# Kernel tuning notes

Hardware: AMD Instinct MI355X
Metric: run time of the kernel (lower is better)

The kernel has to match this reference:

```python
import jax, jax.numpy as jnp
import numpy as np

B, N, F, A = 8, 2048, 512, 512  # batch, n_dim (tokens), feature_dim, attention_dim
BN_EPS = 1e-5


def setup_inputs() -> dict:
    key = jax.random.key(0)
    ks = jax.random.split(key, 9)
    s_f = 1.0 / np.sqrt(F)
    s_a = 1.0 / np.sqrt(A)
    return {
        "x": jax.random.normal(ks[0], (B, N, F), dtype=jnp.float32),
        "Wq": jax.random.uniform(ks[1], (A, F), jnp.float32, -s_f, s_f),
        "bq": jax.random.uniform(ks[2], (A,), jnp.float32, -s_f, s_f),
        "Wk": jax.random.uniform(ks[3], (A, F), jnp.float32, -s_f, s_f),
        "bk": jax.random.uniform(ks[4], (A,), jnp.float32, -s_f, s_f),
        "Wv": jax.random.uniform(ks[5], (A, F), jnp.float32, -s_f, s_f),
        "bv": jax.random.uniform(ks[6], (A,), jnp.float32, -s_f, s_f),
        "Wo": jax.random.uniform(ks[7], (F, A), jnp.float32, -s_a, s_a),
        "bo": jax.random.uniform(ks[8], (F,), jnp.float32, -s_a, s_a),
        "gamma": jnp.ones((N,), dtype=jnp.float32),
        "beta": jnp.zeros((N,), dtype=jnp.float32),
    }


def reference(x, Wq, bq, Wk, bk, Wv, bv, Wo, bo, gamma, beta):
    # QKV projections: [B,N,F] -> [B,N,A]
    q = jnp.einsum("bnf,af->bna", x, Wq) + bq
    k = jnp.einsum("bnf,af->bna", x, Wk) + bk
    v = jnp.einsum("bnf,af->bna", x, Wv) + bv
    # unscaled single-head attention (no 1/sqrt(d) factor, matches source)
    scores = jnp.einsum("bna,bma->bnm", q, k)          # [B,N,N]
    weights = jax.nn.softmax(scores, axis=-1)
    feature = jnp.einsum("bnm,bma->bna", weights, v)    # [B,N,A]
    # LBR: Linear -> BatchNorm1d(n_dim) over channel dim N -> ReLU
    lin = jnp.einsum("bna,fa->bnf", feature, Wo) + bo   # [B,N,F]
    mean = jnp.mean(lin, axis=(0, 2), keepdims=True)    # stats over batch+last dim
    var = jnp.mean(jnp.square(lin - mean), axis=(0, 2), keepdims=True)  # biased var
    bn = gamma[None, :, None] * (lin - mean) * jax.lax.rsqrt(var + BN_EPS) + beta[None, :, None]
    return jax.nn.relu(bn) + x
```

## Files before the change

### kernel.cpp

```cpp
#include <hip/hip_runtime.h>
#include <hip/hip_fp16.h>
#include <stdint.h>

#define B_   8
#define N_   2048
#define F_   512
#define A_   512
#define MTOT (B_ * N_)

typedef unsigned short u16;
typedef unsigned int   u32;
typedef __attribute__((ext_vector_type(8))) __bf16    bf16x8;
typedef __attribute__((ext_vector_type(8))) _Float16  f16x8;
typedef __attribute__((ext_vector_type(4))) float     f32x4;

__device__ __forceinline__ u16 f2bf(float f) {
    u32 u = __builtin_bit_cast(u32, f);
    u32 r = u + 0x7fffu + ((u >> 16) & 1u);
    return (u16)(r >> 16);
}
__device__ __forceinline__ float bf2f(u16 h) {
    return __builtin_bit_cast(float, (u32)h << 16);
}
__device__ __forceinline__ u16 f2h(float f) {
    _Float16 h = (_Float16)f;
    return __builtin_bit_cast(u16, h);
}

__device__ __forceinline__ void gload_lds16(const u16* g, u16* l) {
    __builtin_amdgcn_global_load_lds(
        (const __attribute__((address_space(1))) u32*)(const u32*)g,
        (__attribute__((address_space(3))) u32*)(u32*)l,
        16, 0, 0);
}

#define VMCNT(n) asm volatile("s_waitcnt vmcnt(" #n ")" ::: "memory")
#define LGKM0()  asm volatile("s_waitcnt lgkmcnt(0)" ::: "memory")
#define SCHEDB() __builtin_amdgcn_sched_barrier(0)

__device__ __forceinline__ void sync_pre() {
    SCHEDB();
    __builtin_amdgcn_s_barrier();
    LGKM0();
    SCHEDB();
}
__device__ __forceinline__ void sync_post() {
    SCHEDB();
    __builtin_amdgcn_s_barrier();
}

__global__ __launch_bounds__(256) void cvt_x(const float* __restrict__ in,
                                             u16* __restrict__ out, int n4) {
    int i = blockIdx.x * 256 + threadIdx.x;
    if (i >= n4) return;
    float4 v = ((const float4*)in)[i];
    u32 a = (u32)f2h(v.x) | ((u32)f2h(v.y) << 16);
    u32 b = (u32)f2h(v.z) | ((u32)f2h(v.w) << 16);
    ((uint2*)out)[i] = make_uint2(a, b);
}

__global__ __launch_bounds__(256)
void cvt_wb(const float* __restrict__ Wq, const float* __restrict__ Wk,
            const float* __restrict__ Wv, const float* __restrict__ Wo,
            const float* __restrict__ bq, const float* __restrict__ bk,
            u16* __restrict__ wqkh, u16* __restrict__ wvh, u16* __restrict__ wob,
            float* __restrict__ bqk)
{
    int b = blockIdx.x, t = threadIdx.x;
    int i = (b & 255) * 256 + t;
    int seg = b >> 8;
    const float* src = seg == 0 ? Wq : seg == 1 ? Wk : seg == 2 ? Wv : Wo;
    u16* dst = seg == 0 ? wqkh : seg == 1 ? (wqkh + 262144) : seg == 2 ? wvh : wob;
    float4 v = ((const float4*)src)[i];
    u32 a, c;
    if (seg < 3) {
        a = (u32)f2h(v.x) | ((u32)f2h(v.y) << 16);
        c = (u32)f2h(v.z) | ((u32)f2h(v.w) << 16);
    } else {
        a = (u32)f2bf(v.x) | ((u32)f2bf(v.y) << 16);
        c = (u32)f2bf(v.z) | ((u32)f2bf(v.w) << 16);
    }
    ((uint2*)dst)[i] = make_uint2(a, c);
    if (b == 0 && t < 128) ((float4*)bqk)[t]         = ((const float4*)bq)[t];
    if (b == 1 && t < 128) ((float4*)(bqk + 512))[t] = ((const float4*)bk)[t];
}

template <int BN, int BIAS_MODE, int OUT_FMT, int IN_FMT, int EPI, int XS>
__global__ __launch_bounds__(512, 2)
void gemm8(const u16* __restrict__ A, int lda, long sA,
           const u16* __restrict__ Bm, int ldb, long sB,
           const float* __restrict__ bias,
           void* __restrict__ Cv, int ldc, long sC, int K, int bdiag,
           float* __restrict__ aux)
{
    constexpr int UNITS = (BN == 256) ? 4 : 3;
    constexpr int NF = BN / 64;
    __shared__ alignas(16) u16 lds[2 * UNITS * 8192];

    int bx = blockIdx.x, bz = blockIdx.z;
    if constexpr (XS == 1) { int tt = bx; bx = bz; bz = tt; }
    if constexpr (XS == 2) { bx = ((bx & 7) << 3) | (bx >> 3); }
    const int z  = bz;
    const int m0 = bx * 256;
    const int n0 = blockIdx.y * BN;
    const u16* Ag = A  + (long)z * sA + (long)m0 * lda;
    const u16* Bg = Bm + (long)z * sB + (long)n0 * ldb + (long)(m0 >> 11) * bdiag;

    const int t = threadIdx.x;
    const int lane = t & 63;
    const int wave = t >> 6;
    const int wm = wave >> 2, wn = wave & 3;
    const int frow = lane & 15;
    const int fk8 = (lane >> 4) * 8;

    const int srr = t >> 3;
    const int ses = ((t & 7) * 8) ^ ((srr & 7) << 3);

    auto stageA = [&](int buf, int h, int kt) {
        u16* dst = &lds[(buf * UNITS + h) * 8192 + t * 8];
        const u16* g = Ag + kt * 64 + ses;
        gload_lds16(g + (long)(srr + h * 64) * lda,        dst);
        gload_lds16(g + (long)(srr + 128 + h * 64) * lda,  dst + 4096);
    };
    auto stageB = [&](int buf, int h, int kt) {
        u16* dst = &lds[(buf * UNITS + 2 + h) * 8192 + t * 8];
        const u16* g = Bg + kt * 64 + ses;
        int R0;
        if constexpr (BN == 256) R0 = (srr & 31) + ((srr >> 5) << 6) + h * 32;
        else                     R0 = srr;
        int R1 = R0 + ((BN == 256) ? 128 : 64);
        gload_lds16(g + (long)R0 * ldb, dst);
        gload_lds16(g + (long)R1 * ldb, dst + 4096);
    };
    auto rdA = [&](int buf, int q, int i, int ks) -> uint4 {
        int rr = wm * 64 + i * 16 + frow;
        int e  = (ks * 32 + fk8) ^ ((rr & 7) << 3);
        return *(const uint4*)&lds[(buf * UNITS + q) * 8192 + rr * 64 + e];
    };
    auto rdB = [&](int buf, int p, int j, int ks) -> uint4 {
        int rr = wn * 32 + j * 16 + frow;
        int e  = (ks * 32 + fk8) ^ ((rr & 7) << 3);
        return *(const uint4*)&lds[(buf * UNITS + 2 + p) * 8192 + rr * 64 + e];
    };
    auto MF = [&](uint4 a, uint4 b, f32x4 c) -> f32x4 {
        if constexpr (IN_FMT == 0)
            return __builtin_amdgcn_mfma_f32_16x16x32_bf16(
                __builtin_bit_cast(bf16x8, a), __builtin_bit_cast(bf16x8, b), c, 0, 0, 0);
        else
            return __builtin_amdgcn_mfma_f32_16x16x32_f16(
                __builtin_bit_cast(f16x8, a), __builtin_bit_cast(f16x8, b), c, 0, 0, 0);
    };

    f32x4 acc[8][NF];
#pragma unroll
    for (int i = 0; i < 8; i++)
#pragma unroll
        for (int j = 0; j < NF; j++)
#pragma unroll
            for (int r = 0; r < 4; r++) acc[i][j][r] = 0.f;

    uint4 fa[4][2], fb0[2][2], fb1[2][2];
    const int NT = K >> 6;

    if constexpr (BN == 256) {
        stageA(0, 0, 0); stageB(0, 0, 0); stageB(0, 1, 0); stageA(0, 1, 0);
        VMCNT(4);
    } else {
        stageA(0, 0, 0); stageB(0, 0, 0); stageA(0, 1, 0);
        VMCNT(2);
    }
    SCHEDB();
    __builtin_amdgcn_s_barrier();

    for (int kt = 0; kt < NT; ++kt) {
        const int buf = kt & 1, nb = buf ^ 1;
        const bool st = (kt + 1 < NT);

        if constexpr (BN == 256) {
#pragma unroll
            for (int i = 0; i < 4; i++) { fa[i][0] = rdA(buf, 0, i, 0); fa[i][1] = rdA(buf, 0, i, 1); }
#pragma unroll
            for (int j = 0; j < 2; j++) { fb0[j][0] = rdB(buf, 0, j, 0); fb0[j][1] = rdB(buf, 0, j, 1); }
            if (st) { stageA(nb, 0, kt + 1); VMCNT(4); } else VMCNT(2);
            sync_pre();
            __builtin_amdgcn_s_setprio(1);
#pragma unroll
            for (int ks = 0; ks < 2; ks++)
#pragma unroll
                for (int i = 0; i < 4; i++)
#pragma unroll
                    for (int j = 0; j < 2; j++)
                        acc[i][j] = MF(fa[i][ks], fb0[j][ks], acc[i][j]);
            __builtin_amdgcn_s_setprio(0);
            sync_post();
#pragma unroll
            for (int j = 0; j < 2; j++) { fb1[j][0] = rdB(buf, 1, j, 0); fb1[j][1] = rdB(buf, 1, j, 1); }
            if (st) { stageB(nb, 0, kt + 1); VMCNT(4); } else VMCNT(0);
            sync_pre();
            __builtin_amdgcn_s_setprio(1);
#pragma unroll
            for (int ks = 0; ks < 2; ks++)
#pragma unroll
                for (int i = 0; i < 4; i++)
#pragma unroll
                    for (int j = 0; j < 2; j++)
                        acc[i][2 + j] = MF(fa[i][ks], fb1[j][ks], acc[i][2 + j]);
            __builtin_amdgcn_s_setprio(0);
            sync_post();
#pragma unroll
            for (int i = 0; i < 4; i++) { fa[i][0] = rdA(buf, 1, i, 0); fa[i][1] = rdA(buf, 1, i, 1); }
            if (st) stageB(nb, 1, kt + 1);
            sync_pre();
            __builtin_amdgcn_s_setprio(1);
#pragma unroll
            for (int ks = 0; ks < 2; ks++)
#pragma unroll
                for (int i = 0; i < 4; i++)
#pragma unroll
                    for (int j = 0; j < 2; j++)
                        acc[4 + i][j] = MF(fa[i][ks], fb0[j][ks], acc[4 + i][j]);
            __builtin_amdgcn_s_setprio(0);
            sync_post();
            if (st) { stageA(nb, 1, kt + 1); VMCNT(4); }
            sync_pre();
            __builtin_amdgcn_s_setprio(1);
#pragma unroll
            for (int ks = 0; ks < 2; ks++)
#pragma unroll
                for (int i = 0; i < 4; i++)
#pragma unroll
                    for (int j = 0; j < 2; j++)
                        acc[4 + i][2 + j] = MF(fa[i][ks], fb1[j][ks], acc[4 + i][2 + j]);
            __builtin_amdgcn_s_setprio(0);
            sync_post();
        } else {
#pragma unroll
            for (int i = 0; i < 4; i++) { fa[i][0] = rdA(buf, 0, i, 0); fa[i][1] = rdA(buf, 0, i, 1); }
#pragma unroll
            for (int j = 0; j < 2; j++) { fb0[j][0] = rdB(buf, 0, j, 0); fb0[j][1] = rdB(buf, 0, j, 1); }
            if (st) { stageA(nb, 0, kt + 1); stageB(nb, 0, kt + 1); VMCNT(4); } else VMCNT(0);
            sync_pre();
            __builtin_amdgcn_s_setprio(1);
#pragma unroll
            for (int ks = 0; ks < 2; ks++)
#pragma unroll
                for (int i = 0; i < 4; i++)
#pragma unroll
                    for (int j = 0; j < 2; j++)
                        acc[i][j] = MF(fa[i][ks], fb0[j][ks], acc[i][j]);
            __builtin_amdgcn_s_setprio(0);
            sync_post();
#pragma unroll
            for (int i = 0; i < 4; i++) { fa[i][0] = rdA(buf, 1, i, 0); fa[i][1] = rdA(buf, 1, i, 1); }
            if (st) { stageA(nb, 1, kt + 1); VMCNT(2); }
            sync_pre();
            __builtin_amdgcn_s_setprio(1);
#pragma unroll
            for (int ks = 0; ks < 2; ks++)
#pragma unroll
                for (int i = 0; i < 4; i++)
#pragma unroll
                    for (int j = 0; j < 2; j++)
                        acc[4 + i][j] = MF(fa[i][ks], fb0[j][ks], acc[4 + i][j]);
            __builtin_amdgcn_s_setprio(0);
            sync_post();
        }
    }

    const int rq = (lane >> 4) * 4;
#pragma unroll
    for (int am = 0; am < 8; am++) {
        const int m = m0 + wm * 128 + (am >> 2) * 64 + (am & 3) * 16 + rq;
#pragma unroll
        for (int r = 0; r < 4; r++) {
            float rscale = 1.f;
            if constexpr (EPI == 3) rscale = 1.0f / aux[m + r];
            float se = 0.f, s1 = 0.f, s2 = 0.f;
#pragma unroll
            for (int an = 0; an < NF; an++) {
                const int n = n0 + wn * (BN / 4) + an * 16 + frow;
                float v = acc[am][an][r];
                if (BIAS_MODE == 1) v += bias[n];
                if (BIAS_MODE == 2) v += bias[m + r];
                if constexpr (EPI == 1) { v = __expf(v); se += v; }
                if constexpr (EPI == 3) { v *= rscale; }
                if constexpr (EPI == 2) { s1 += v; s2 += v * v; }
                long idx = (long)(m + r) * ldc + n + (long)z * sC;
                if constexpr (OUT_FMT == 0)      ((u16*)Cv)[idx] = f2bf(v);
                else if constexpr (OUT_FMT == 1) ((float*)Cv)[idx] = v;
                else                             ((u16*)Cv)[idx] = f2h(v);
            }
            if constexpr (EPI == 1) {
#pragma unroll
                for (int o = 1; o < 16; o <<= 1) se += __shfl_xor(se, o);
                if (frow == 0)
                    atomicAdd(&aux[(long)z * N_ + m + r], se);
            }
            if constexpr (EPI == 2) {
#pragma unroll
                for (int o = 1; o < 16; o <<= 1) { s1 += __shfl_xor(s1, o); s2 += __shfl_xor(s2, o); }
                if (frow == 0) {
                    int tok = (m + r) & (N_ - 1);
                    atomicAdd(&aux[tok], s1);
                    atomicAdd(&aux[N_ + tok], s2);
                }
            }
        }
    }
}

__global__ __launch_bounds__(256)
void bn_relu_add(const u16* __restrict__ linb, const u16* __restrict__ xh,
                 const float* __restrict__ gamma, const float* __restrict__ beta,
                 const float* __restrict__ stats, float* __restrict__ out) {
    long i4 = (long)blockIdx.x * 256 + threadIdx.x;
    int n = (int)((i4 >> 7) & (N_ - 1));
    float mean = stats[n] * (1.f / 4096.f);
    float var  = stats[N_ + n] * (1.f / 4096.f) - mean * mean;
    float rstd = rsqrtf(var + 1e-5f);
    float scale = gamma[n] * rstd;
    float shift = beta[n] - mean * scale;
    uint2 lb = ((const uint2*)linb)[i4];
    uint2 xb = ((const uint2*)xh)[i4];
    float2 x01 = __half22float2(__builtin_bit_cast(__half2, xb.x));
    float2 x23 = __half22float2(__builtin_bit_cast(__half2, xb.y));
    float4 o;
    o.x = fmaxf(bf2f((u16)lb.x)         * scale + shift, 0.f) + x01.x;
    o.y = fmaxf(bf2f((u16)(lb.x >> 16)) * scale + shift, 0.f) + x01.y;
    o.z = fmaxf(bf2f((u16)lb.y)         * scale + shift, 0.f) + x23.x;
    o.w = fmaxf(bf2f((u16)(lb.y >> 16)) * scale + shift, 0.f) + x23.y;
    ((float4*)out)[i4] = o;
}

extern "C" void kernel_launch(void* const* d_in, const int* in_sizes, int n_in,
                              void* d_out, int out_size, void* d_ws, size_t ws_size,
                              hipStream_t stream)
{
    (void)in_sizes; (void)n_in; (void)out_size; (void)ws_size;
    const float* x     = (const float*)d_in[0];
    const float* Wq    = (const float*)d_in[1];
    const float* bq    = (const float*)d_in[2];
    const float* Wk    = (const float*)d_in[3];
    const float* bk    = (const float*)d_in[4];
    const float* Wv    = (const float*)d_in[5];
    const float* bv    = (const float*)d_in[6];
    const float* Wo    = (const float*)d_in[7];
    const float* bo    = (const float*)d_in[8];
    const float* gamma = (const float*)d_in[9];
    const float* beta  = (const float*)d_in[10];
    float* out = (float*)d_out;
    char*  ws  = (char*)d_ws;

    const size_t MB = 1024 * 1024;
    u16*   wqkh  = (u16*)(ws + 0);
    u16*   wvh   = (u16*)(ws + 1 * MB);
    u16*   wob   = (u16*)(ws + 1 * MB + 512 * 1024);
    float* stats = (float*)(ws + 2 * MB);
    float* rowsum= (float*)(ws + 2 * MB + 16 * 1024);
    float* bqk   = (float*)(ws + 2 * MB + 80 * 1024);
    u16*   xh    = (u16*)(ws + 4 * MB);
    u16*   qkh   = (u16*)(ws + 20 * MB);
    u16*   vt    = (u16*)(ws + 52 * MB);
    u16*   P     = (u16*)(ws + 68 * MB);
    u16*   feat  = (u16*)(ws + 132 * MB);
    u16*   lin   = (u16*)(ws + 148 * MB);

    hipMemsetAsync(stats, 0, 80 * 1024, stream);

    cvt_x<<<8192, 256, 0, stream>>>(x, xh, 2097152);
    cvt_wb<<<1024, 256, 0, stream>>>(Wq, Wk, Wv, Wo, bq, bk, wqkh, wvh, wob, bqk);

    gemm8<256, 1, 2, 1, 0, 0><<<dim3(64, 4, 1), 512, 0, stream>>>(
        xh, 512, 0, wqkh, 512, 0, bqk, qkh, 1024, 0, 512, 0, nullptr);
    gemm8<128, 2, 0, 1, 0, 0><<<dim3(2, 128, 1), 512, 0, stream>>>(
        wvh, 512, 0, xh, 512, 0, bv, vt, MTOT, 0, 512, 0, nullptr);
    gemm8<256, 0, 0, 1, 1, 1><<<dim3(8, 8, 8), 512, 0, stream>>>(
        qkh, 1024, (long)N_ * 1024, qkh + 512, 1024, (long)N_ * 1024,
        nullptr, P, N_, (long)N_ * N_, 512, 0, rowsum);
    gemm8<128, 0, 0, 0, 3, 2><<<dim3(64, 4, 1), 512, 0, stream>>>(
        P, N_, 0, vt, MTOT, 0, nullptr, feat, A_, 0, 2048, 2048, rowsum);
    gemm8<128, 1, 0, 0, 2, 0><<<dim3(64, 4, 1), 512, 0, stream>>>(
        feat, 512, 0, wob, 512, 0, bo, lin, 512, 0, 512, 0, stats);

    bn_relu_add<<<8192, 256, 0, stream>>>(lin, xh, gamma, beta, stats, out);
}
```

Baseline: 217.2 us.

## Replace GEMM double-buffer with triple-buffered 256x128 tile pipeline

Replaces the gemm8 template (BN 256 or 128, double-buffered LDS, two barriers per sub-step) with gemm9, which uses only 256x128 tiles and a three-stage LDS ring that prefetches two k-steps ahead. Each k-iteration now needs one barrier instead of several, which is meant to cut sync overhead and hide global-load latency. The QK projection and score GEMMs move from BN=256 to BN=128 with twice the grid in y. That loses some A-tile reuse, and the larger LDS footprint (144KB) plus the dropped min-blocks launch bound reduce occupancy to one block per CU.

```diff
diff --git a/kernel.cpp b/kernel.cpp
--- a/kernel.cpp
+++ b/kernel.cpp
@@ -37,17 +37,6 @@
 #define VMCNT(n) asm volatile("s_waitcnt vmcnt(" #n ")" ::: "memory")
 #define LGKM0()  asm volatile("s_waitcnt lgkmcnt(0)" ::: "memory")
 #define SCHEDB() __builtin_amdgcn_sched_barrier(0)
-
-__device__ __forceinline__ void sync_pre() {
-    SCHEDB();
-    __builtin_amdgcn_s_barrier();
-    LGKM0();
-    SCHEDB();
-}
-__device__ __forceinline__ void sync_post() {
-    SCHEDB();
-    __builtin_amdgcn_s_barrier();
-}
 
 __global__ __launch_bounds__(256) void cvt_x(const float* __restrict__ in,
                                              u16* __restrict__ out, int n4) {
@@ -85,24 +74,22 @@
     if (b == 1 && t < 128) ((float4*)(bqk + 512))[t] = ((const float4*)bk)[t];
 }
 
-template <int BN, int BIAS_MODE, int OUT_FMT, int IN_FMT, int EPI, int XS>
-__global__ __launch_bounds__(512, 2)
-void gemm8(const u16* __restrict__ A, int lda, long sA,
+template <int BIAS_MODE, int OUT_FMT, int IN_FMT, int EPI, int XS>
+__global__ __launch_bounds__(512)
+void gemm9(const u16* __restrict__ A, int lda, long sA,
            const u16* __restrict__ Bm, int ldb, long sB,
            const float* __restrict__ bias,
            void* __restrict__ Cv, int ldc, long sC, int K, int bdiag,
            float* __restrict__ aux)
 {
-    constexpr int UNITS = (BN == 256) ? 4 : 3;
-    constexpr int NF = BN / 64;
-    __shared__ alignas(16) u16 lds[2 * UNITS * 8192];
+    __shared__ alignas(16) u16 lds[9 * 8192];
 
     int bx = blockIdx.x, bz = blockIdx.z;
     if constexpr (XS == 1) { int tt = bx; bx = bz; bz = tt; }
     if constexpr (XS == 2) { bx = ((bx & 7) << 3) | (bx >> 3); }
     const int z  = bz;
     const int m0 = bx * 256;
-    const int n0 = blockIdx.y * BN;
+    const int n0 = blockIdx.y * 128;
     const u16* Ag = A  + (long)z * sA + (long)m0 * lda;
     const u16* Bg = Bm + (long)z * sB + (long)n0 * ldb + (long)(m0 >> 11) * bdiag;
 
@@ -117,30 +104,26 @@
     const int ses = ((t & 7) * 8) ^ ((srr & 7) << 3);
 
     auto stageA = [&](int buf, int h, int kt) {
-        u16* dst = &lds[(buf * UNITS + h) * 8192 + t * 8];
+        u16* dst = &lds[(buf * 3 + h) * 8192 + t * 8];
         const u16* g = Ag + kt * 64 + ses;
         gload_lds16(g + (long)(srr + h * 64) * lda,        dst);
         gload_lds16(g + (long)(srr + 128 + h * 64) * lda,  dst + 4096);
     };
-    auto stageB = [&](int buf, int h, int kt) {
-        u16* dst = &lds[(buf * UNITS + 2 + h) * 8192 + t * 8];
+    auto stageB = [&](int buf, int kt) {
+        u16* dst = &lds[(buf * 3 + 2) * 8192 + t * 8];
         const u16* g = Bg + kt * 64 + ses;
-        int R0;
-        if constexpr (BN == 256) R0 = (srr & 31) + ((srr >> 5) << 6) + h * 32;
-        else                     R0 = srr;
-        int R1 = R0 + ((BN == 256) ? 128 : 64);
-        gload_lds16(g + (long)R0 * ldb, dst);
-        gload_lds16(g + (long)R1 * ldb, dst + 4096);
+        gload_lds16(g + (long)srr * ldb,        dst);
+        gload_lds16(g + (long)(srr + 64) * ldb, dst + 4096);
     };
     auto rdA = [&](int buf, int q, int i, int ks) -> uint4 {
         int rr = wm * 64 + i * 16 + frow;
         int e  = (ks * 32 + fk8) ^ ((rr & 7) << 3);
-        return *(const uint4*)&lds[(buf * UNITS + q) * 8192 + rr * 64 + e];
-    };
-    auto rdB = [&](int buf, int p, int j, int ks) -> uint4 {
+        return *(const uint4*)&lds[(buf * 3 + q) * 8192 + rr * 64 + e];
+    };
+    auto rdB = [&](int buf, int j, int ks) -> uint4 {
         int rr = wn * 32 + j * 16 + frow;
         int e  = (ks * 32 + fk8) ^ ((rr & 7) << 3);
-        return *(const uint4*)&lds[(buf * UNITS + 2 + p) * 8192 + rr * 64 + e];
+        return *(const uint4*)&lds[(buf * 3 + 2) * 8192 + rr * 64 + e];
     };
     auto MF = [&](uint4 a, uint4 b, f32x4 c) -> f32x4 {
         if constexpr (IN_FMT == 0)
@@ -151,120 +134,62 @@
                 __builtin_bit_cast(f16x8, a), __builtin_bit_cast(f16x8, b), c, 0, 0, 0);
     };
 
-    f32x4 acc[8][NF];
+    f32x4 acc[8][2];
 #pragma unroll
     for (int i = 0; i < 8; i++)
 #pragma unroll
-        for (int j = 0; j < NF; j++)
+        for (int j = 0; j < 2; j++)
 #pragma unroll
             for (int r = 0; r < 4; r++) acc[i][j][r] = 0.f;
 
-    uint4 fa[4][2], fb0[2][2], fb1[2][2];
+    uint4 fa[4][2], fb[2][2];
     const int NT = K >> 6;
 
-    if constexpr (BN == 256) {
-        stageA(0, 0, 0); stageB(0, 0, 0); stageB(0, 1, 0); stageA(0, 1, 0);
-        VMCNT(4);
-    } else {
-        stageA(0, 0, 0); stageB(0, 0, 0); stageA(0, 1, 0);
-        VMCNT(2);
-    }
-    SCHEDB();
-    __builtin_amdgcn_s_barrier();
-
+    stageA(0, 0, 0); stageB(0, 0); stageA(0, 1, 0);
+    stageA(1, 0, 1); stageB(1, 1); stageA(1, 1, 1);
+
+    int bR = 0;
     for (int kt = 0; kt < NT; ++kt) {
-        const int buf = kt & 1, nb = buf ^ 1;
-        const bool st = (kt + 1 < NT);
-
-        if constexpr (BN == 256) {
-#pragma unroll
-            for (int i = 0; i < 4; i++) { fa[i][0] = rdA(buf, 0, i, 0); fa[i][1] = rdA(buf, 0, i, 1); }
-#pragma unroll
-            for (int j = 0; j < 2; j++) { fb0[j][0] = rdB(buf, 0, j, 0); fb0[j][1] = rdB(buf, 0, j, 1); }
-            if (st) { stageA(nb, 0, kt + 1); VMCNT(4); } else VMCNT(2);
-            sync_pre();
-            __builtin_amdgcn_s_setprio(1);
-#pragma unroll
-            for (int ks = 0; ks < 2; ks++)
-#pragma unroll
-                for (int i = 0; i < 4; i++)
-#pragma unroll
-                    for (int j = 0; j < 2; j++)
-                        acc[i][j] = MF(fa[i][ks], fb0[j][ks], acc[i][j]);
-            __builtin_amdgcn_s_setprio(0);
-            sync_post();
-#pragma unroll
-            for (int j = 0; j < 2; j++) { fb1[j][0] = rdB(buf, 1, j, 0); fb1[j][1] = rdB(buf, 1, j, 1); }
-            if (st) { stageB(nb, 0, kt + 1); VMCNT(4); } else VMCNT(0);
-            sync_pre();
-            __builtin_amdgcn_s_setprio(1);
-#pragma unroll
-            for (int ks = 0; ks < 2; ks++)
-#pragma unroll
-                for (int i = 0; i < 4; i++)
-#pragma unroll
-                    for (int j = 0; j < 2; j++)
-                        acc[i][2 + j] = MF(fa[i][ks], fb1[j][ks], acc[i][2 + j]);
-            __builtin_amdgcn_s_setprio(0);
-            sync_post();
-#pragma unroll
-            for (int i = 0; i < 4; i++) { fa[i][0] = rdA(buf, 1, i, 0); fa[i][1] = rdA(buf, 1, i, 1); }
-            if (st) stageB(nb, 1, kt + 1);
-            sync_pre();
-            __builtin_amdgcn_s_setprio(1);
-#pragma unroll
-            for (int ks = 0; ks < 2; ks++)
-#pragma unroll
-                for (int i = 0; i < 4; i++)
-#pragma unroll
-                    for (int j = 0; j < 2; j++)
-                        acc[4 + i][j] = MF(fa[i][ks], fb0[j][ks], acc[4 + i][j]);
-            __builtin_amdgcn_s_setprio(0);
-            sync_post();
-            if (st) { stageA(nb, 1, kt + 1); VMCNT(4); }
-            sync_pre();
-            __builtin_amdgcn_s_setprio(1);
-#pragma unroll
-            for (int ks = 0; ks < 2; ks++)
-#pragma unroll
-                for (int i = 0; i < 4; i++)
-#pragma unroll
-                    for (int j = 0; j < 2; j++)
-                        acc[4 + i][2 + j] = MF(fa[i][ks], fb1[j][ks], acc[4 + i][2 + j]);
-            __builtin_amdgcn_s_setprio(0);
-            sync_post();
-        } else {
-#pragma unroll
-            for (int i = 0; i < 4; i++) { fa[i][0] = rdA(buf, 0, i, 0); fa[i][1] = rdA(buf, 0, i, 1); }
-#pragma unroll
-            for (int j = 0; j < 2; j++) { fb0[j][0] = rdB(buf, 0, j, 0); fb0[j][1] = rdB(buf, 0, j, 1); }
-            if (st) { stageA(nb, 0, kt + 1); stageB(nb, 0, kt + 1); VMCNT(4); } else VMCNT(0);
-            sync_pre();
-            __builtin_amdgcn_s_setprio(1);
-#pragma unroll
-            for (int ks = 0; ks < 2; ks++)
-#pragma unroll
-                for (int i = 0; i < 4; i++)
-#pragma unroll
-                    for (int j = 0; j < 2; j++)
-                        acc[i][j] = MF(fa[i][ks], fb0[j][ks], acc[i][j]);
-            __builtin_amdgcn_s_setprio(0);
-            sync_post();
-#pragma unroll
-            for (int i = 0; i < 4; i++) { fa[i][0] = rdA(buf, 1, i, 0); fa[i][1] = rdA(buf, 1, i, 1); }
-            if (st) { stageA(nb, 1, kt + 1); VMCNT(2); }
-            sync_pre();
-            __builtin_amdgcn_s_setprio(1);
-#pragma unroll
-            for (int ks = 0; ks < 2; ks++)
-#pragma unroll
-                for (int i = 0; i < 4; i++)
-#pragma unroll
-                    for (int j = 0; j < 2; j++)
-                        acc[4 + i][j] = MF(fa[i][ks], fb0[j][ks], acc[4 + i][j]);
-            __builtin_amdgcn_s_setprio(0);
-            sync_post();
-        }
+        int bS = bR + 2; if (bS >= 3) bS -= 3;
+        const bool st = (kt + 2 < NT);
+
+        if (kt + 1 < NT) { VMCNT(6); } else { VMCNT(0); }
+        SCHEDB();
+        __builtin_amdgcn_s_barrier();
+        SCHEDB();
+
+        if (st) { stageA(bS, 0, kt + 2); stageB(bS, kt + 2); }
+#pragma unroll
+        for (int i = 0; i < 4; i++) { fa[i][0] = rdA(bR, 0, i, 0); fa[i][1] = rdA(bR, 0, i, 1); }
+#pragma unroll
+        for (int j = 0; j < 2; j++) { fb[j][0] = rdB(bR, j, 0); fb[j][1] = rdB(bR, j, 1); }
+        LGKM0(); SCHEDB();
+        __builtin_amdgcn_s_setprio(1);
+#pragma unroll
+        for (int ks = 0; ks < 2; ks++)
+#pragma unroll
+            for (int i = 0; i < 4; i++)
+#pragma unroll
+                for (int j = 0; j < 2; j++)
+                    acc[i][j] = MF(fa[i][ks], fb[j][ks], acc[i][j]);
+        __builtin_amdgcn_s_setprio(0);
+
+        if (st) stageA(bS, 1, kt + 2);
+#pragma unroll
+        for (int i = 0; i < 4; i++) { fa[i][0] = rdA(bR, 1, i, 0); fa[i][1] = rdA(bR, 1, i, 1); }
+        LGKM0(); SCHEDB();
+        __builtin_amdgcn_s_setprio(1);
+#pragma unroll
+        for (int ks = 0; ks < 2; ks++)
+#pragma unroll
+            for (int i = 0; i < 4; i++)
+#pragma unroll
+                for (int j = 0; j < 2; j++)
+                    acc[4 + i][j] = MF(fa[i][ks], fb[j][ks], acc[4 + i][j]);
+        __builtin_amdgcn_s_setprio(0);
+        SCHEDB();
+
+        bR += 1; if (bR == 3) bR = 0;
     }
 
     const int rq = (lane >> 4) * 4;
@@ -277,8 +202,8 @@
             if constexpr (EPI == 3) rscale = 1.0f / aux[m + r];
             float se = 0.f, s1 = 0.f, s2 = 0.f;
 #pragma unroll
-            for (int an = 0; an < NF; an++) {
-                const int n = n0 + wn * (BN / 4) + an * 16 + frow;
+            for (int an = 0; an < 2; an++) {
+                const int n = n0 + wn * 32 + an * 16 + frow;
                 float v = acc[am][an][r];
                 if (BIAS_MODE == 1) v += bias[n];
                 if (BIAS_MODE == 2) v += bias[m + r];
@@ -370,16 +295,16 @@
     cvt_x<<<8192, 256, 0, stream>>>(x, xh, 2097152);
     cvt_wb<<<1024, 256, 0, stream>>>(Wq, Wk, Wv, Wo, bq, bk, wqkh, wvh, wob, bqk);
 
-    gemm8<256, 1, 2, 1, 0, 0><<<dim3(64, 4, 1), 512, 0, stream>>>(
+    gemm9<1, 2, 1, 0, 0><<<dim3(64, 8, 1), 512, 0, stream>>>(
         xh, 512, 0, wqkh, 512, 0, bqk, qkh, 1024, 0, 512, 0, nullptr);
-    gemm8<128, 2, 0, 1, 0, 0><<<dim3(2, 128, 1), 512, 0, stream>>>(
+    gemm9<2, 0, 1, 0, 0><<<dim3(2, 128, 1), 512, 0, stream>>>(
         wvh, 512, 0, xh, 512, 0, bv, vt, MTOT, 0, 512, 0, nullptr);
-    gemm8<256, 0, 0, 1, 1, 1><<<dim3(8, 8, 8), 512, 0, stream>>>(
+    gemm9<0, 0, 1, 1, 1><<<dim3(8, 16, 8), 512, 0, stream>>>(
         qkh, 1024, (long)N_ * 1024, qkh + 512, 1024, (long)N_ * 1024,
         nullptr, P, N_, (long)N_ * N_, 512, 0, rowsum);
-    gemm8<128, 0, 0, 0, 3, 2><<<dim3(64, 4, 1), 512, 0, stream>>>(
+    gemm9<0, 0, 0, 3, 2><<<dim3(64, 4, 1), 512, 0, stream>>>(
         P, N_, 0, vt, MTOT, 0, nullptr, feat, A_, 0, 2048, 2048, rowsum);
-    gemm8<128, 1, 0, 0, 2, 0><<<dim3(64, 4, 1), 512, 0, stream>>>(
+    gemm9<1, 0, 0, 2, 0><<<dim3(64, 4, 1), 512, 0, stream>>>(
         feat, 512, 0, wob, 512, 0, bo, lin, 512, 0, 512, 0, stats);
 
     bn_relu_add<<<8192, 256, 0, stream>>>(lin, xh, gamma, beta, stats, out);
```

Measured after the change: 294.6 us. +35.6%, slower.

## Add dedicated QK^T kernel computing two N-tiles per block with A reuse

Applied to the files above, without the earlier changes.

Replaces the generic gemm8 instantiation for the attention scores with a specialized kernel where each block covers 256 query rows and two consecutive 256-wide key tiles (512 columns). It streams 16 K-steps, flushing exp(scores) and atomic row sums after each 256-column tile and zeroing the accumulators. The grid halves in the N dimension (8x4x8 = 256 blocks), which lengthens per-block work and cuts launch and prologue overhead. The Q tile is still re-fetched for each key tile, so data reuse changes only slightly, while halving the block count may reduce wave occupancy across CUs.

```diff
diff --git a/kernel.cpp b/kernel.cpp
--- a/kernel.cpp
+++ b/kernel.cpp
@@ -98,7 +98,6 @@
     __shared__ alignas(16) u16 lds[2 * UNITS * 8192];
 
     int bx = blockIdx.x, bz = blockIdx.z;
-    if constexpr (XS == 1) { int tt = bx; bx = bz; bz = tt; }
     if constexpr (XS == 2) { bx = ((bx & 7) << 3) | (bx >> 3); }
     const int z  = bz;
     const int m0 = bx * 256;
@@ -275,14 +274,13 @@
         for (int r = 0; r < 4; r++) {
             float rscale = 1.f;
             if constexpr (EPI == 3) rscale = 1.0f / aux[m + r];
-            float se = 0.f, s1 = 0.f, s2 = 0.f;
+            float s1 = 0.f, s2 = 0.f;
 #pragma unroll
             for (int an = 0; an < NF; an++) {
                 const int n = n0 + wn * (BN / 4) + an * 16 + frow;
                 float v = acc[am][an][r];
                 if (BIAS_MODE == 1) v += bias[n];
                 if (BIAS_MODE == 2) v += bias[m + r];
-                if constexpr (EPI == 1) { v = __expf(v); se += v; }
                 if constexpr (EPI == 3) { v *= rscale; }
                 if constexpr (EPI == 2) { s1 += v; s2 += v * v; }
                 long idx = (long)(m + r) * ldc + n + (long)z * sC;
@@ -290,12 +288,6 @@
                 else if constexpr (OUT_FMT == 1) ((float*)Cv)[idx] = v;
                 else                             ((u16*)Cv)[idx] = f2h(v);
             }
-            if constexpr (EPI == 1) {
-#pragma unroll
-                for (int o = 1; o < 16; o <<= 1) se += __shfl_xor(se, o);
-                if (frow == 0)
-                    atomicAdd(&aux[(long)z * N_ + m + r], se);
-            }
             if constexpr (EPI == 2) {
 #pragma unroll
                 for (int o = 1; o < 16; o <<= 1) { s1 += __shfl_xor(s1, o); s2 += __shfl_xor(s2, o); }
@@ -303,6 +295,159 @@
                     int tok = (m + r) & (N_ - 1);
                     atomicAdd(&aux[tok], s1);
                     atomicAdd(&aux[N_ + tok], s2);
+                }
+            }
+        }
+    }
+}
+
+__global__ __launch_bounds__(512, 2)
+void gemm_qk(const u16* __restrict__ qk, u16* __restrict__ P,
+             float* __restrict__ rowsum)
+{
+    __shared__ alignas(16) u16 lds[2 * 4 * 8192];
+
+    const int z  = blockIdx.x;
+    const int m0 = blockIdx.z * 256;
+    const int n0b = blockIdx.y * 512;
+    const u16* Ag  = qk + (long)z * N_ * 1024 + (long)m0 * 1024;
+    const u16* Bgb = qk + 512 + (long)z * N_ * 1024;
+
+    const int t = threadIdx.x;
+    const int lane = t & 63;
+    const int wave = t >> 6;
+    const int wm = wave >> 2, wn = wave & 3;
+    const int frow = lane & 15;
+    const int fk8 = (lane >> 4) * 8;
+
+    const int srr = t >> 3;
+    const int ses = ((t & 7) * 8) ^ ((srr & 7) << 3);
+
+    auto stageA = [&](int buf, int h, int tt) {
+        u16* dst = &lds[(buf * 4 + h) * 8192 + t * 8];
+        const u16* g = Ag + (tt & 7) * 64 + ses;
+        gload_lds16(g + (long)(srr + h * 64) * 1024,        dst);
+        gload_lds16(g + (long)(srr + 128 + h * 64) * 1024,  dst + 4096);
+    };
+    auto stageB = [&](int buf, int h, int tt) {
+        u16* dst = &lds[(buf * 4 + 2 + h) * 8192 + t * 8];
+        const u16* g = Bgb + (long)(n0b + (tt >> 3) * 256) * 1024 + (tt & 7) * 64 + ses;
+        int R0 = (srr & 31) + ((srr >> 5) << 6) + h * 32;
+        gload_lds16(g + (long)R0 * 1024,         dst);
+        gload_lds16(g + (long)(R0 + 128) * 1024, dst + 4096);
+    };
+    auto rdA = [&](int buf, int q, int i, int ks) -> uint4 {
+        int rr = wm * 64 + i * 16 + frow;
+        int e  = (ks * 32 + fk8) ^ ((rr & 7) << 3);
+        return *(const uint4*)&lds[(buf * 4 + q) * 8192 + rr * 64 + e];
+    };
+    auto rdB = [&](int buf, int p, int j, int ks) -> uint4 {
+        int rr = wn * 32 + j * 16 + frow;
+        int e  = (ks * 32 + fk8) ^ ((rr & 7) << 3);
+        return *(const uint4*)&lds[(buf * 4 + 2 + p) * 8192 + rr * 64 + e];
+    };
+    auto MF = [&](uint4 a, uint4 b, f32x4 c) -> f32x4 {
+        return __builtin_amdgcn_mfma_f32_16x16x32_f16(
+            __builtin_bit_cast(f16x8, a), __builtin_bit_cast(f16x8, b), c, 0, 0, 0);
+    };
+
+    f32x4 acc[8][4];
+#pragma unroll
+    for (int i = 0; i < 8; i++)
+#pragma unroll
+        for (int j = 0; j < 4; j++)
+#pragma unroll
+            for (int r = 0; r < 4; r++) acc[i][j][r] = 0.f;
+
+    uint4 fa[4][2], fb0[2][2], fb1[2][2];
+    const int rq = (lane >> 4) * 4;
+
+    stageA(0, 0, 0); stageB(0, 0, 0); stageB(0, 1, 0); stageA(0, 1, 0);
+    VMCNT(4);
+    SCHEDB();
+    __builtin_amdgcn_s_barrier();
+
+    for (int tt = 0; tt < 16; ++tt) {
+        const int buf = tt & 1, nb = buf ^ 1;
+        const bool st = (tt + 1 < 16);
+
+#pragma unroll
+        for (int i = 0; i < 4; i++) { fa[i][0] = rdA(buf, 0, i, 0); fa[i][1] = rdA(buf, 0, i, 1); }
+#pragma unroll
+        for (int j = 0; j < 2; j++) { fb0[j][0] = rdB(buf, 0, j, 0); fb0[j][1] = rdB(buf, 0, j, 1); }
+        if (st) { stageA(nb, 0, tt + 1); VMCNT(4); } else VMCNT(2);
+        sync_pre();
+        __builtin_amdgcn_s_setprio(1);
+#pragma unroll
+        for (int ks = 0; ks < 2; ks++)
+#pragma unroll
+            for (int i = 0; i < 4; i++)
+#pragma unroll
+                for (int j = 0; j < 2; j++)
+                    acc[i][j] = MF(fa[i][ks], fb0[j][ks], acc[i][j]);
+        __builtin_amdgcn_s_setprio(0);
+        sync_post();
+#pragma unroll
+        for (int j = 0; j < 2; j++) { fb1[j][0] = rdB(buf, 1, j, 0); fb1[j][1] = rdB(buf, 1, j, 1); }
+        if (st) { stageB(nb, 0, tt + 1); VMCNT(4); } else VMCNT(0);
+        sync_pre();
+        __builtin_amdgcn_s_setprio(1);
+#pragma unroll
+        for (int ks = 0; ks < 2; ks++)
+#pragma unroll
+            for (int i = 0; i < 4; i++)
+#pragma unroll
+                for (int j = 0; j < 2; j++)
+                    acc[i][2 + j] = MF(fa[i][ks], fb1[j][ks], acc[i][2 + j]);
+        __builtin_amdgcn_s_setprio(0);
+        sync_post();
+#pragma unroll
+        for (int i = 0; i < 4; i++) { fa[i][0] = rdA(buf, 1, i, 0); fa[i][1] = rdA(buf, 1, i, 1); }
+        if (st) stageB(nb, 1, tt + 1);
+        sync_pre();
+        __builtin_amdgcn_s_setprio(1);
+#pragma unroll
+        for (int ks = 0; ks < 2; ks++)
+#pragma unroll
+            for (int i = 0; i < 4; i++)
+#pragma unroll
+                for (int j = 0; j < 2; j++)
+                    acc[4 + i][j] = MF(fa[i][ks], fb0[j][ks], acc[4 + i][j]);
+        __builtin_amdgcn_s_setprio(0);
+        sync_post();
+        if (st) { stageA(nb, 1, tt + 1); VMCNT(4); }
+        sync_pre();
+        __builtin_amdgcn_s_setprio(1);
+#pragma unroll
+        for (int ks = 0; ks < 2; ks++)
+#pragma unroll
+            for (int i = 0; i < 4; i++)
+#pragma unroll
+                for (int j = 0; j < 2; j++)
+                    acc[4 + i][2 + j] = MF(fa[i][ks], fb1[j][ks], acc[4 + i][2 + j]);
+        __builtin_amdgcn_s_setprio(0);
+        sync_post();
+
+        if ((tt & 7) == 7) {
+            const int n0 = n0b + (tt >> 3) * 256;
+#pragma unroll
+            for (int am = 0; am < 8; am++) {
+                const int m = m0 + wm * 128 + (am >> 2) * 64 + (am & 3) * 16 + rq;
+#pragma unroll
+                for (int r = 0; r < 4; r++) {
+                    float se = 0.f;
+#pragma unroll
+                    for (int an = 0; an < 4; an++) {
+                        const int n = n0 + wn * 64 + an * 16 + frow;
+                        float v = __expf(acc[am][an][r]);
+                        se += v;
+                        P[(long)z * N_ * N_ + (long)(m + r) * N_ + n] = f2bf(v);
+                        acc[am][an][r] = 0.f;
+                    }
+#pragma unroll
+                    for (int o = 1; o < 16; o <<= 1) se += __shfl_xor(se, o);
+                    if (frow == 0)
+                        atomicAdd(&rowsum[(long)z * N_ + m + r], se);
                 }
             }
         }
@@ -374,9 +519,7 @@
         xh, 512, 0, wqkh, 512, 0, bqk, qkh, 1024, 0, 512, 0, nullptr);
     gemm8<128, 2, 0, 1, 0, 0><<<dim3(2, 128, 1), 512, 0, stream>>>(
         wvh, 512, 0, xh, 512, 0, bv, vt, MTOT, 0, 512, 0, nullptr);
-    gemm8<256, 0, 0, 1, 1, 1><<<dim3(8, 8, 8), 512, 0, stream>>>(
-        qkh, 1024, (long)N_ * 1024, qkh + 512, 1024, (long)N_ * 1024,
-        nullptr, P, N_, (long)N_ * N_, 512, 0, rowsum);
+    gemm_qk<<<dim3(8, 4, 8), 512, 0, stream>>>(qkh, P, rowsum);
     gemm8<128, 0, 0, 0, 3, 2><<<dim3(64, 4, 1), 512, 0, stream>>>(
         P, N_, 0, vt, MTOT, 0, nullptr, feat, A_, 0, 2048, 2048, rowsum);
     gemm8<128, 1, 0, 0, 2, 0><<<dim3(64, 4, 1), 512, 0, stream>>>(
```

New measurement: 222.2 us. +2.3%, slower.
